# Optimization experiments

Measured on AMD Instinct MI355X. Metric: run time of the kernel, lower is better.

Reference implementation:

```python
import jax, jax.numpy as jnp
import numpy as np

P_ITER = 30   # Krylov iterations (p_iter=30 in source)
N_PROBE = 100 # stochastic probe vectors (t=100 in source)


def setup_inputs() -> dict:
    N, t, r = 8192, N_PROBE, 256
    key = jax.random.key(0)
    kA, ky, kz = jax.random.split(key, 3)
    # Well-conditioned SPD kernel + noise matrix: K = A A^T / r + I
    A = jax.random.normal(kA, (N, r), dtype=jnp.float32)
    Knn_noise = (A @ A.T) / r + jnp.eye(N, dtype=jnp.float32)
    y = jax.random.normal(ky, (N, 1), dtype=jnp.float32)
    # Rademacher probes (||z||^2 = N exactly)
    Z = jnp.where(jax.random.normal(kz, (N, t)) >= 0, 1.0, -1.0).astype(jnp.float32)
    return {"Knn_noise": Knn_noise, "y": y, "Z": Z}


def _batched_cg(K, B, p_iter):
    """Batched conjugate gradients on K X = B, tracking Lanczos coefficients.
    B: [N, M]. Returns X [N, M], alphas [p, M], betas [p, M]."""
    X = jnp.zeros_like(B)
    R = B
    P = B
    rs = jnp.sum(R * R, axis=0)  # [M]

    def step(carry, _):
        X, R, P, rs = carry
        V = K @ P                               # [N, M] dense matvec (GEMM)
        pv = jnp.sum(P * V, axis=0)             # [M]
        alpha = rs / pv
        X = X + alpha * P
        R = R - alpha * V
        rs_new = jnp.sum(R * R, axis=0)
        beta = rs_new / rs
        P = R + beta * P
        return (X, R, P, rs_new), (alpha, beta)

    (X, _, _, _), (alphas, betas) = jax.lax.scan(step, (X, R, P, rs), None, length=p_iter)
    return X, alphas, betas


def _slq_logdet(alphas, betas, N):
    """Stochastic Lanczos quadrature logdet from CG coefficients.
    alphas, betas: [p, t] (one column per probe)."""
    inv_a = 1.0 / alphas                                   # [p, t]
    diag = inv_a.at[1:].add(betas[:-1] / alphas[:-1])      # T diagonal  [p, t]
    off = jnp.sqrt(betas[:-1]) / alphas[:-1]               # T off-diag  [p-1, t]

    def make_T(d, o):
        return jnp.diag(d) + jnp.diag(o, 1) + jnp.diag(o, -1)

    Ts = jax.vmap(make_T, in_axes=(1, 1))(diag, off)       # [t, p, p]
    lam, V = jnp.linalg.eigh(Ts)                           # small p x p eig per probe
    lam = jnp.maximum(lam, 1e-12)
    # z^T log(K) z ~= ||z||^2 * e1^T Vexp log(Lam) V^T e1 ; ||z||^2 = N (Rademacher)
    quad = jnp.sum(V[:, 0, :] ** 2 * jnp.log(lam), axis=1)  # [t]
    return N * jnp.mean(quad)


def reference(Knn_noise, y, Z):
    N = y.shape[0]
    B = jnp.concatenate([y, Z], axis=1)                    # solve + probes together
    X, alphas, betas = _batched_cg(Knn_noise, B, P_ITER)
    Knn_i_y = X[:, :1]                                     # K^{-1} y
    log_det = _slq_logdet(alphas[:, 1:], betas[:, 1:], N)  # SLQ logdet from probes
    two_pi = jnp.asarray(2.0 * np.pi, dtype=y.dtype)
    return -0.5 * (y.T @ Knn_i_y) - 0.5 * log_det - N * 0.5 * jnp.log(two_pi)
```

## Files before the change

### kernel.cpp

```cpp
#include <hip/hip_runtime.h>
#include <hip/hip_bf16.h>

#define NN 8192
#define NCOLS 101
#define CPW 112
#define CPAD 128
#define BM 64
#define KSPL 4
#define KCH (NN / KSPL)
#define NSTEP (KCH / 128)
#define PITER 30
#define PVLD 104

typedef __attribute__((ext_vector_type(4))) float f32x4;

__device__ __forceinline__ void async_copy16(const void* g, void* l) {
  __builtin_amdgcn_global_load_lds(
      (const __attribute__((address_space(1))) unsigned int*)g,
      (__attribute__((address_space(3))) unsigned int*)l, 16, 0, 0);
}

__device__ __forceinline__ unsigned int pack_fp8x4(float x, float y, float z, float w) {
  unsigned int v = __builtin_amdgcn_cvt_pk_fp8_f32(x, y, 0, false);
  v = __builtin_amdgcn_cvt_pk_fp8_f32(z, w, v, true);
  return v;
}

__device__ __forceinline__ float block_sum(float v) {
  #pragma unroll
  for (int o = 32; o > 0; o >>= 1) v += __shfl_down(v, o);
  __shared__ float sw[4];
  int w = threadIdx.x >> 6;
  if ((threadIdx.x & 63) == 0) sw[w] = v;
  __syncthreads();
  float r = 0.f;
  if (threadIdx.x < 4) r = sw[threadIdx.x];
  r += __shfl_down(r, 2);
  r += __shfl_down(r, 1);
  return r;
}

__global__ __launch_bounds__(256, 2) void gemm_kernel(
    const unsigned char* __restrict__ Kb,
    const unsigned char* __restrict__ Pb,
    const float* __restrict__ Pf,
    const float* __restrict__ SCit,
    float* __restrict__ Vp,
    float* __restrict__ pvp) {
  __shared__ __align__(16) unsigned char sA[BM * 128];
  __shared__ __align__(16) unsigned char sB[CPAD * 128];
  __shared__ __align__(16) float sC[BM * 113];

  int bx = blockIdx.x;
  int rb = bx & 127;
  int kz = bx >> 7;
  int tid = threadIdx.x;
  int lane = tid & 63;
  int w = tid >> 6;
  int r0 = rb * BM;
  int k0 = kz * KCH;
  int lrow = lane >> 3;
  int lseg = lane & 7;
  int gseg = lseg ^ lrow;
  int mm = lane & 15;
  int quad = lane >> 4;

  f32x4 acc[7];
  #pragma unroll
  for (int i = 0; i < 7; ++i) acc[i] = (f32x4){0.f, 0.f, 0.f, 0.f};

  for (int s = 0; s < NSTEP; ++s) {
    int kk = k0 + s * 128;
    #pragma unroll
    for (int q = 0; q < 2; ++q) {
      int rl = w * 16 + q * 8 + lrow;
      async_copy16(Kb + (size_t)(r0 + rl) * NN + kk + gseg * 16,
                   (char*)sA + (size_t)(w * 16 + q * 8) * 128);
    }
    #pragma unroll
    for (int q = 0; q < 4; ++q) {
      int cl = w * 32 + q * 8 + lrow;
      async_copy16(Pb + (size_t)cl * NN + kk + gseg * 16,
                   (char*)sB + (size_t)(w * 32 + q * 8) * 128);
    }
    __syncthreads();
    int arow = w * 16 + mm;
    #pragma unroll
    for (int kh = 0; kh < 4; ++kh) {
      int seg16 = kh * 2 + (quad >> 1);
      long long aF = *(const long long*)(sA + arow * 128 +
                     ((seg16 ^ (arow & 7)) << 4) + ((quad & 1) << 3));
      #pragma unroll
      for (int ct = 0; ct < 7; ++ct) {
        int bcol = ct * 16 + mm;
        long long bF = *(const long long*)(sB + bcol * 128 +
                       ((seg16 ^ (bcol & 7)) << 4) + ((quad & 1) << 3));
        acc[ct] = __builtin_amdgcn_mfma_f32_16x16x32_fp8_fp8(aF, bF, acc[ct], 0, 0, 0);
      }
    }
    __syncthreads();
  }
  #pragma unroll
  for (int ct = 0; ct < 7; ++ct)
    #pragma unroll
    for (int r = 0; r < 4; ++r)
      sC[(w * 16 + quad * 4 + r) * 113 + ct * 16 + mm] = acc[ct][r];
  __syncthreads();
  float* Vout = Vp + (size_t)kz * ((size_t)CPW * NN);
  for (int idx = tid; idx < BM * CPW; idx += 256) {
    int col = idx >> 6;
    int row = idx & 63;
    if (col < NCOLS)
      Vout[(size_t)col * NN + r0 + row] = sC[row * 113 + col] * SCit[col];
  }
  int rr = tid & 63;
  int g = tid >> 6;
  for (int j = 0; j < 28; ++j) {
    int c = g + j * 4;
    float prod = 0.f;
    if (c < NCOLS)
      prod = sC[rr * 113 + c] * SCit[c] * Pf[(size_t)c * NN + r0 + rr];
    #pragma unroll
    for (int o = 32; o > 0; o >>= 1) prod += __shfl_down(prod, o);
    if (rr == 0 && c < NCOLS) pvp[(size_t)bx * PVLD + c] = prod;
  }
}

__global__ void update1_kernel(const float* __restrict__ Vp,
                               const float* __restrict__ Pf,
                               float* __restrict__ R,
                               float* __restrict__ X0,
                               const float* __restrict__ pvp,
                               const float* __restrict__ rs,
                               float* __restrict__ rs_new,
                               float* __restrict__ alphas) {
  const size_t SPL = (size_t)CPW * NN;
  __shared__ float s_alpha;
  int c = blockIdx.y;
  int t = threadIdx.x;
  float pvv = pvp[(size_t)t * PVLD + c] + pvp[(size_t)(t + 256) * PVLD + c];
  float pvtot = block_sum(pvv);
  if (t == 0) s_alpha = rs[c] / pvtot;
  __syncthreads();
  float alpha = s_alpha;

  size_t off = (size_t)c * NN + blockIdx.x * 1024 + t * 4;
  float4 a = *(const float4*)(Vp + off);
  float4 b = *(const float4*)(Vp + SPL + off);
  float4 d = *(const float4*)(Vp + 2 * SPL + off);
  float4 e = *(const float4*)(Vp + 3 * SPL + off);
  float4 v;
  v.x = a.x + b.x + d.x + e.x;
  v.y = a.y + b.y + d.y + e.y;
  v.z = a.z + b.z + d.z + e.z;
  v.w = a.w + b.w + d.w + e.w;
  float4 r = *(float4*)(R + off);
  r.x -= alpha * v.x; r.y -= alpha * v.y; r.z -= alpha * v.z; r.w -= alpha * v.w;
  *(float4*)(R + off) = r;
  if (c == 0) {
    size_t xo = blockIdx.x * 1024 + t * 4;
    float4 x = *(float4*)(X0 + xo);
    float4 p = *(const float4*)(Pf + off);
    x.x += alpha * p.x; x.y += alpha * p.y; x.z += alpha * p.z; x.w += alpha * p.w;
    *(float4*)(X0 + xo) = x;
  }
  float rn = r.x * r.x + r.y * r.y + r.z * r.z + r.w * r.w;
  float tot = block_sum(rn);
  if (t == 0) {
    atomicAdd(rs_new + c, tot);
    if (blockIdx.x == 0) alphas[c] = alpha;
  }
}

__global__ void update2_kernel(const float* __restrict__ R,
                               float* __restrict__ P,
                               unsigned char* __restrict__ Pb,
                               const float* __restrict__ rs,
                               const float* __restrict__ rs_new,
                               const float* __restrict__ PNold,
                               float* __restrict__ PNnew,
                               float* __restrict__ SCnew,
                               float* __restrict__ betas) {
  int c = blockIdx.y;
  float rsn = rs_new[c];
  float beta = rsn / rs[c];
  float pnn = rsn + beta * beta * PNold[c];
  float sc = exp2f(roundf(0.5f * log2f(pnn * (1.f / 8192.f))));
  float inv = 1.f / sc;
  size_t off = (size_t)c * NN + blockIdx.x * 1024 + threadIdx.x * 4;
  float4 r = *(const float4*)(R + off);
  float4 p = *(float4*)(P + off);
  p.x = r.x + beta * p.x; p.y = r.y + beta * p.y;
  p.z = r.z + beta * p.z; p.w = r.w + beta * p.w;
  *(float4*)(P + off) = p;
  *(unsigned int*)(Pb + off) = pack_fp8x4(p.x * inv, p.y * inv, p.z * inv, p.w * inv);
  if (threadIdx.x == 0 && blockIdx.x == 0) {
    betas[c] = beta;
    PNnew[c] = pnn;
    SCnew[c] = sc;
  }
}

__global__ void cast_k_kernel(const float* __restrict__ K, unsigned char* __restrict__ Kb) {
  size_t i = ((size_t)blockIdx.x * 256 + threadIdx.x) * 4;
  size_t stride = (size_t)gridDim.x * 1024;
  for (; i < (size_t)NN * NN; i += stride) {
    float4 f = *(const float4*)(K + i);
    *(unsigned int*)(Kb + i) = pack_fp8x4(f.x, f.y, f.z, f.w);
  }
}

__global__ void init_vec_kernel(const float* __restrict__ y, const float* __restrict__ Z,
                                float* __restrict__ P, float* __restrict__ R,
                                unsigned char* __restrict__ Pb) {
  int c = blockIdx.y;
  int i = blockIdx.x * 256 + threadIdx.x;
  float val = (c == 0) ? y[i] : Z[(size_t)i * 100 + (c - 1)];
  size_t off = (size_t)c * NN + i;
  P[off] = val;
  R[off] = val;
  Pb[off] = (unsigned char)(__builtin_amdgcn_cvt_pk_fp8_f32(val, 0.f, 0, false) & 0xFF);
}

#define NSMALL 23424
__global__ void init_misc_kernel(float* __restrict__ X0, float* __restrict__ smalls,
                                 unsigned char* __restrict__ Pbpad) {
  const int total = 8192 + NSMALL + 27 * NN;
  for (int t = blockIdx.x * 256 + threadIdx.x; t < total; t += gridDim.x * 256) {
    if (t < 8192) X0[t] = 0.f;
    else if (t < 8192 + NSMALL) smalls[t - 8192] = 0.f;
    else Pbpad[t - (8192 + NSMALL)] = 0;
  }
}

__global__ void init_rs_kernel(const float* __restrict__ y, float* __restrict__ rs0,
                               float* __restrict__ pn0, float* __restrict__ sc0) {
  int t = threadIdx.x;
  float s = 0.f;
  for (int i = t; i < NN; i += 256) { float v = y[i]; s += v * v; }
  float tot = block_sum(s);
  if (t == 0) { rs0[0] = tot; pn0[0] = tot; }
  if (t >= 1 && t <= 100) { rs0[t] = (float)NN; pn0[t] = (float)NN; }
  if (t < 128) sc0[t] = 1.f;
}

__global__ __launch_bounds__(64, 1) void slq_kernel(
    const float* __restrict__ AL, const float* __restrict__ BE,
    float* __restrict__ QP) {
  __shared__ double sd[PITER], se[PITER];
  int lane = threadIdx.x;
  int c = blockIdx.x + 1;
  if (lane < PITER) {
    double a = (double)AL[lane * 128 + c];
    double dd = 1.0 / a;
    if (lane > 0) {
      double ap = (double)AL[(lane - 1) * 128 + c];
      double bp = (double)BE[(lane - 1) * 128 + c];
      dd += bp / ap;
    }
    sd[lane] = dd;
    double ee = 0.0;
    if (lane < PITER - 1) {
      double b = (double)BE[lane * 128 + c];
      ee = sqrt(b) / a;
    }
    se[lane] = ee;
  }
  __syncthreads();
  double d[PITER], e[PITER];
  #pragma unroll
  for (int i = 0; i < PITER; ++i) { d[i] = sd[i]; e[i] = se[i]; }

  float quadk = 0.f;
  if (lane < PITER) {
    double lo = 1e300, hi = -1e300;
    #pragma unroll
    for (int i = 0; i < PITER; ++i) {
      double r = e[i] + (i > 0 ? e[i - 1] : 0.0);
      lo = fmin(lo, d[i] - r);
      hi = fmax(hi, d[i] + r);
    }
    int k = lane;
    for (int it = 0; it < 48; ++it) {
      double mid = 0.5 * (lo + hi);
      int cnt = 0;
      double q = d[0] - mid;
      cnt += (q < 0.0);
      #pragma unroll
      for (int i = 1; i < PITER; ++i) {
        double aq = fabs(q);
        if (aq < 1e-30) q = (q < 0.0) ? -1e-30 : 1e-30;
        q = d[i] - mid - (e[i - 1] * e[i - 1]) / q;
        cnt += (q < 0.0);
      }
      if (cnt > k) hi = mid; else lo = mid;
    }
    double lam = 0.5 * (lo + hi);
    double e0 = fmax(e[0], 1e-150);
    double vprev = 1.0;
    double vcur = (lam - d[0]) / e0;
    double s = 1.0 + vcur * vcur;
    double scale2 = 1.0;
    #pragma unroll
    for (int i = 1; i < PITER - 1; ++i) {
      double ei = fmax(e[i], 1e-150);
      double vnext = ((lam - d[i]) * vcur - e[i - 1] * vprev) / ei;
      if (fabs(vnext) > 1e150) {
        vnext *= 1e-150; vcur *= 1e-150; s *= 1e-300; scale2 *= 1e-300;
      }
      vprev = vcur; vcur = vnext;
      s += vcur * vcur;
    }
    double w = scale2 / s;
    double lc = lam > 1e-12 ? lam : 1e-12;
    quadk = (float)(w * log(lc));
  }
  #pragma unroll
  for (int o = 32; o > 0; o >>= 1) quadk += __shfl_down(quadk, o);
  if (lane == 0) QP[blockIdx.x] = quadk;
}

__global__ void final2_kernel(const float* __restrict__ y, const float* __restrict__ X0,
                              const float* __restrict__ QP, float* __restrict__ out) {
  int t = threadIdx.x;
  float s = 0.f;
  for (int i = t; i < NN; i += 256) s += y[i] * X0[i];
  float ydot = block_sum(s);
  __syncthreads();
  float q = (t < 100) ? QP[t] : 0.f;
  float qsum = block_sum(q);
  if (t == 0) {
    float logdet = (float)NN * (qsum * 0.01f);
    out[0] = -0.5f * ydot - 0.5f * logdet - (float)NN * 0.5f * 1.8378770664093454f;
  }
}

extern "C" void kernel_launch(void* const* d_in, const int* in_sizes, int n_in,
                              void* d_out, int out_size, void* d_ws, size_t ws_size,
                              hipStream_t stream) {
  const float* K = (const float*)d_in[0];
  const float* y = (const float*)d_in[1];
  const float* Z = (const float*)d_in[2];
  float* out = (float*)d_out;
  char* ws = (char*)d_ws;
  if (ws_size < 89796096ull) return;

  unsigned char* Kb = (unsigned char*)(ws + 0ull);
  unsigned char* Pb = (unsigned char*)(ws + 67108864ull);
  float* P   = (float*)(ws + 68157440ull);
  float* R   = (float*)(ws + 71467008ull);
  float* Vp  = (float*)(ws + 74776576ull);
  float* X0  = (float*)(ws + 89456640ull);
  float* PVP = (float*)(ws + 89489408ull);
  float* SM  = (float*)(ws + 89702400ull);
  float* RS = SM;
  float* AL = SM + 7808;
  float* BE = SM + 11648;
  float* PN = SM + 15488;
  float* SC = SM + 19456;
  float* QP = Vp;

  cast_k_kernel<<<8192, 256, 0, stream>>>(K, Kb);
  init_vec_kernel<<<dim3(32, 101), 256, 0, stream>>>(y, Z, P, R, Pb);
  init_misc_kernel<<<240, 256, 0, stream>>>(X0, SM, Pb + (size_t)NCOLS * NN);
  init_rs_kernel<<<1, 256, 0, stream>>>(y, RS, PN, SC);

  for (int it = 0; it < PITER; ++it) {
    gemm_kernel<<<512, 256, 0, stream>>>(Kb, Pb, P, SC + it * 128, Vp, PVP);
    update1_kernel<<<dim3(8, 101), 256, 0, stream>>>(Vp, P, R, X0, PVP,
        RS + it * 128, RS + (it + 1) * 128, AL + it * 128);
    update2_kernel<<<dim3(8, 101), 256, 0, stream>>>(R, P, Pb, RS + it * 128,
        RS + (it + 1) * 128, PN + it * 128, PN + (it + 1) * 128,
        SC + (it + 1) * 128, BE + it * 128);
  }
  slq_kernel<<<100, 64, 0, stream>>>(AL, BE, QP);
  final2_kernel<<<1, 256, 0, stream>>>(y, X0, QP, out);
}
```

Before: 2.043 ms.

## Double-buffer LDS tiles in fp8 GEMM to overlap async loads with MFMA

Splits shared memory into two buffers for the K and P tiles. The next k-step's global_load_lds copies are issued before the current step's MFMA work, so global memory latency overlaps with compute. The C staging area now aliases the operand buffers in one 48KB block, which keeps total LDS near its old size. This relies on the end-of-loop barrier draining the async copies and on the last iteration finishing before sC overwrites the operand buffers.

```diff
diff --git a/kernel.cpp b/kernel.cpp
--- a/kernel.cpp
+++ b/kernel.cpp
@@ -47,9 +47,10 @@
     const float* __restrict__ SCit,
     float* __restrict__ Vp,
     float* __restrict__ pvp) {
-  __shared__ __align__(16) unsigned char sA[BM * 128];
-  __shared__ __align__(16) unsigned char sB[CPAD * 128];
-  __shared__ __align__(16) float sC[BM * 113];
+  __shared__ __align__(16) unsigned char smem[49152];
+  unsigned char* sA = smem;
+  unsigned char* sB = smem + 16384;
+  float* sC = (float*)smem;
 
   int bx = blockIdx.x;
   int rb = bx & 127;
@@ -60,8 +61,7 @@
   int r0 = rb * BM;
   int k0 = kz * KCH;
   int lrow = lane >> 3;
-  int lseg = lane & 7;
-  int gseg = lseg ^ lrow;
+  int gseg = (lane & 7) ^ lrow;
   int mm = lane & 15;
   int quad = lane >> 4;
 
@@ -69,31 +69,39 @@
   #pragma unroll
   for (int i = 0; i < 7; ++i) acc[i] = (f32x4){0.f, 0.f, 0.f, 0.f};
 
+  auto stage = [&](int s, int buf) {
+    int kk = k0 + s * 128;
+    #pragma unroll
+    for (int q = 0; q < 2; ++q) {
+      async_copy16(Kb + (size_t)(r0 + w * 16 + q * 8 + lrow) * NN + kk + gseg * 16,
+                   sA + buf * 8192 + (w * 16 + q * 8) * 128);
+    }
+    #pragma unroll
+    for (int q = 0; q < 4; ++q) {
+      async_copy16(Pb + (size_t)(w * 32 + q * 8 + lrow) * NN + kk + gseg * 16,
+                   sB + buf * 16384 + (w * 32 + q * 8) * 128);
+    }
+  };
+
+  stage(0, 0);
+  __syncthreads();
+
+  int arow = w * 16 + mm;
+  #pragma unroll 2
   for (int s = 0; s < NSTEP; ++s) {
-    int kk = k0 + s * 128;
-    #pragma unroll
-    for (int q = 0; q < 2; ++q) {
-      int rl = w * 16 + q * 8 + lrow;
-      async_copy16(Kb + (size_t)(r0 + rl) * NN + kk + gseg * 16,
-                   (char*)sA + (size_t)(w * 16 + q * 8) * 128);
-    }
-    #pragma unroll
-    for (int q = 0; q < 4; ++q) {
-      int cl = w * 32 + q * 8 + lrow;
-      async_copy16(Pb + (size_t)cl * NN + kk + gseg * 16,
-                   (char*)sB + (size_t)(w * 32 + q * 8) * 128);
-    }
-    __syncthreads();
-    int arow = w * 16 + mm;
+    int cur = s & 1;
+    if (s + 1 < NSTEP) stage(s + 1, cur ^ 1);
+    const unsigned char* A = sA + cur * 8192;
+    const unsigned char* B = sB + cur * 16384;
     #pragma unroll
     for (int kh = 0; kh < 4; ++kh) {
       int seg16 = kh * 2 + (quad >> 1);
-      long long aF = *(const long long*)(sA + arow * 128 +
+      long long aF = *(const long long*)(A + arow * 128 +
                      ((seg16 ^ (arow & 7)) << 4) + ((quad & 1) << 3));
       #pragma unroll
       for (int ct = 0; ct < 7; ++ct) {
         int bcol = ct * 16 + mm;
-        long long bF = *(const long long*)(sB + bcol * 128 +
+        long long bF = *(const long long*)(B + bcol * 128 +
                        ((seg16 ^ (bcol & 7)) << 4) + ((quad & 1) << 3));
         acc[ct] = __builtin_amdgcn_mfma_f32_16x16x32_fp8_fp8(aF, bF, acc[ct], 0, 0, 0);
       }
```

Result: faster. 1.901 ms (-7.0%).
